# Performance work log

Measured on AMD Instinct MI355X. Metric: run time of the kernel, lower is better.

The kernel has to match this reference:

```python
import jax, jax.numpy as jnp
import numpy as np

NUM_CODES = 1024
CODE_DIM = 256
COMMIT_W = 0.25
EPS = 1e-5
ENT_LO, ENT_HI = 0.5, 0.9
ENT_W = 0.1
VAR_FLOOR = 0.05
VAR_W = 1e-3
DECORR_W = 1e-3


def setup_inputs() -> dict:
    key = jax.random.key(0)
    k1, k2, k3 = jax.random.split(key, 3)
    inputs = jax.random.normal(k1, (16, 2048, CODE_DIM), dtype=jnp.float32)
    weight = jax.random.normal(k2, (NUM_CODES, CODE_DIM), dtype=jnp.float32) * 0.1
    usage_counts = jax.random.uniform(k3, (NUM_CODES,), dtype=jnp.float32)
    return {"inputs": inputs, "weight": weight, "usage_counts": usage_counts}


def reference(inputs, weight, usage_counts):
    K, D = weight.shape
    flat = inputs.reshape(-1, D)  # [N, D]
    # squared euclidean distances [N, K]
    dist = (flat ** 2).sum(axis=1, keepdims=True) - 2.0 * flat @ weight.T + (weight ** 2).sum(axis=1)
    idx = jnp.argmin(dist, axis=1)  # [N]
    quant = weight[idx].reshape(inputs.shape)

    commitment_loss = COMMIT_W * jnp.mean((jax.lax.stop_gradient(quant) - inputs) ** 2)
    # straight-through estimator
    quant_ste = inputs + jax.lax.stop_gradient(quant - inputs)

    # usage entropy regularizer
    probs = usage_counts + EPS
    probs = probs / jnp.maximum(probs.sum(), EPS * K)
    usage_entropy = -jnp.sum(probs * jnp.log(probs + EPS)) / np.log(float(K)).astype(np.float32)
    gap = jnp.where(usage_entropy < ENT_LO, ENT_LO - usage_entropy,
                    jnp.where(usage_entropy > ENT_HI, usage_entropy - ENT_HI, 0.0))
    entropy_loss = ENT_W * gap ** 2

    # variance floor penalty on codebook
    variance = jnp.var(weight, axis=0)
    variance_loss = VAR_W * jnp.mean(jax.nn.relu(VAR_FLOOR - variance))

    # decorrelation penalty
    wc = weight - weight.mean(axis=0, keepdims=True)
    cov = wc.T @ wc / float(K)  # [D, D]
    off_diag = cov - jnp.diag(jnp.diag(cov))
    decorrelation_loss = DECORR_W * jnp.mean(off_diag ** 2)

    total_loss = commitment_loss + entropy_loss + variance_loss + decorrelation_loss
    indices = idx.reshape(inputs.shape[:-1])
    return (quant_ste, indices, total_loss, commitment_loss, entropy_loss,
            variance_loss, decorrelation_loss, usage_entropy)
```

## Files before the change

kernel.cpp:

```cpp
#include <hip/hip_runtime.h>
#include <math.h>

#define DIMS   256
#define KCODES 1024
#define NTOT   32768
#define TAU    0.002f

typedef __bf16 bf16x8 __attribute__((ext_vector_type(8)));
typedef float  f32x4  __attribute__((ext_vector_type(4)));

typedef const void __attribute__((address_space(1))) glb_cv;
typedef void __attribute__((address_space(3))) lds_v;

__device__ __forceinline__ void gload_lds16(const void* g, void* l) {
  __builtin_amdgcn_global_load_lds((glb_cv*)g, (lds_v*)l, 16, 0, 0);
}

#define WS_COMMIT   0
#define WS_FLAGCNT  1
#define WS_DECORR   2
#define WS_COLSUM   16
#define WS_COLSQ    272
#define WS_WSQ      1024
#define WS_XSQ      2048
#define WS_FLAGS    34816
#define WS_CAND1    67584
#define WS_CAND2    329728
#define WS_CANDI    591872
#define WS_WP       854016

#define OUT_Q    0
#define OUT_IDX  8388608
#define OUT_SCAL 8421376

__global__ __launch_bounds__(256) void pack_kernel(const float* __restrict__ src,
                                                   __bf16* __restrict__ dst,
                                                   float* __restrict__ sqOut) {
  int tid = threadIdx.x;
  int row = blockIdx.x * 64 + (tid >> 2);
  int kg = tid & 3;
  int rb = row >> 7, rl = row & 127;
  int p1 = kg ^ (rl & 7);
  float sq = 0.f;
  #pragma unroll
  for (int kt = 0; kt < 8; kt++) {
    const float* s = src + (size_t)row * DIMS + kt * 32 + kg * 8;
    float4 u = *(const float4*)s;
    float4 v = *(const float4*)(s + 4);
    float f[8] = {u.x, u.y, u.z, u.w, v.x, v.y, v.z, v.w};
    bf16x8 hi, lo;
    #pragma unroll
    for (int e = 0; e < 8; e++) {
      __bf16 h = (__bf16)f[e];
      hi[e] = h;
      lo[e] = (__bf16)(f[e] - (float)h);
      sq = fmaf(f[e], f[e], sq);
    }
    size_t base = ((size_t)(rb * 8 + kt) * 128 + rl) * 64;
    *(bf16x8*)&dst[base + p1 * 8] = hi;
    *(bf16x8*)&dst[base + (p1 ^ 4) * 8] = lo;
  }
  sq += __shfl_xor(sq, 1);
  sq += __shfl_xor(sq, 2);
  if (kg == 0) sqOut[row] = sq;
}

__global__ __launch_bounds__(256) void colstats_kernel(const float* __restrict__ W, float* ws) {
  int d = threadIdx.x;
  int r0 = blockIdx.x * 32;
  float s = 0.f, sq = 0.f;
  #pragma unroll 8
  for (int k = 0; k < 32; k++) {
    float v = W[(size_t)(r0 + k) * DIMS + d];
    s += v;
    sq = fmaf(v, v, sq);
  }
  atomicAdd(&ws[WS_COLSUM + d], s);
  atomicAdd(&ws[WS_COLSQ + d], sq);
}

__global__ __launch_bounds__(256) void pass1_kernel(const __bf16* __restrict__ Xp,
                                                    const __bf16* __restrict__ Wp,
                                                    float* ws) {
  __shared__ __align__(16) char smem[65536];
  __shared__ float wsqs[128];
  float* d1L = (float*)smem;
  float* d2L = (float*)(smem + 1024);
  int*   i1L = (int*)(smem + 2048);

  int tid = threadIdx.x;
  int lane = tid & 63, wave = tid >> 6;
  int waveM = wave >> 1, waveN = wave & 1;
  int quad = lane >> 4, col = lane & 15;
  int l = blockIdx.x;
  int bm = (l & 7) * 32 + ((l >> 3) & 31);
  int bn = l >> 8;
  int rowBase = bm * 128, cb = bn * 128;

  if (tid < 128) wsqs[tid] = ws[WS_WSQ + cb + tid];

  f32x4 acc[4][4];
  #pragma unroll
  for (int i = 0; i < 4; i++)
    #pragma unroll
    for (int j = 0; j < 4; j++) acc[i][j] = (f32x4){0.f, 0.f, 0.f, 0.f};

  const char* abase = (const char*)(Xp + ((size_t)(bm * 8) << 13));
  const char* bbase = (const char*)(Wp + ((size_t)(bn * 8) << 13));
  int llo = wave * 4096 + lane * 16;

  #pragma unroll
  for (int i = 0; i < 4; i++) {
    int off = wave * 4096 + i * 1024;
    gload_lds16(abase + off + lane * 16, smem + off);
    gload_lds16(bbase + off + lane * 16, smem + 32768 + off);
  }
  (void)llo;

  for (int kt = 0; kt < 8; kt++) {
    __syncthreads();
    if (kt < 7) {
      int b = (kt + 1) & 1;
      const char* as = abase + (size_t)(kt + 1) * 16384;
      const char* bs = bbase + (size_t)(kt + 1) * 16384;
      #pragma unroll
      for (int i = 0; i < 4; i++) {
        int off = wave * 4096 + i * 1024;
        gload_lds16(as + off + lane * 16, smem + b * 16384 + off);
        gload_lds16(bs + off + lane * 16, smem + 32768 + b * 16384 + off);
      }
    }
    const __bf16* Ab = (const __bf16*)(smem + (kt & 1) * 16384);
    const __bf16* Bb = (const __bf16*)(smem + 32768 + (kt & 1) * 16384);

    bf16x8 ah[4], al[4];
    #pragma unroll
    for (int mt = 0; mt < 4; mt++) {
      int r = waveM * 64 + mt * 16 + col;
      int ph = quad ^ (r & 7);
      ah[mt] = *(const bf16x8*)&Ab[r * 64 + ph * 8];
      al[mt] = *(const bf16x8*)&Ab[r * 64 + (ph ^ 4) * 8];
    }
    #pragma unroll
    for (int nt = 0; nt < 4; nt++) {
      int r = waveN * 64 + nt * 16 + col;
      int ph = quad ^ (r & 7);
      bf16x8 bh = *(const bf16x8*)&Bb[r * 64 + ph * 8];
      bf16x8 bl = *(const bf16x8*)&Bb[r * 64 + (ph ^ 4) * 8];
      #pragma unroll
      for (int mt = 0; mt < 4; mt++) {
        acc[mt][nt] = __builtin_amdgcn_mfma_f32_16x16x32_bf16(ah[mt], bh, acc[mt][nt], 0, 0, 0);
        acc[mt][nt] = __builtin_amdgcn_mfma_f32_16x16x32_bf16(ah[mt], bl, acc[mt][nt], 0, 0, 0);
        acc[mt][nt] = __builtin_amdgcn_mfma_f32_16x16x32_bf16(al[mt], bh, acc[mt][nt], 0, 0, 0);
      }
    }
  }

  #pragma unroll
  for (int mt = 0; mt < 4; mt++) {
    #pragma unroll
    for (int r = 0; r < 4; r++) {
      float d1 = 3.0e38f, d2 = 3.0e38f;
      int i1 = 0;
      #pragma unroll
      for (int nt = 0; nt < 4; nt++) {
        int lc = waveN * 64 + nt * 16 + col;
        float d = wsqs[lc] - 2.0f * acc[mt][nt][r];
        int g = cb + lc;
        if (d < d1) { d2 = d1; d1 = d; i1 = g; }
        else if (d < d2) d2 = d;
      }
      #pragma unroll
      for (int m = 1; m < 16; m <<= 1) {
        float od1 = __shfl_xor(d1, m);
        int oi1 = __shfl_xor(i1, m);
        float od2 = __shfl_xor(d2, m);
        if (od1 < d1 || (od1 == d1 && oi1 < i1)) {
          d2 = fminf(d1, fminf(d2, od2));
          d1 = od1; i1 = oi1;
        } else {
          d2 = fminf(od1, fminf(d2, od2));
        }
      }
      if (col == 0) {
        int lr = waveM * 64 + mt * 16 + quad * 4 + r;
        d1L[lr * 2 + waveN] = d1;
        d2L[lr * 2 + waveN] = d2;
        i1L[lr * 2 + waveN] = i1;
      }
    }
  }
  __syncthreads();
  if (tid < 128) {
    float a1 = d1L[tid * 2], a2 = d2L[tid * 2];
    int ai = i1L[tid * 2];
    float b1 = d1L[tid * 2 + 1], b2 = d2L[tid * 2 + 1];
    int bi = i1L[tid * 2 + 1];
    float m1, m2; int mi;
    if (b1 < a1 || (b1 == a1 && bi < ai)) { m1 = b1; mi = bi; m2 = fminf(a1, b2); }
    else { m1 = a1; mi = ai; m2 = fminf(b1, a2); }
    int o = bn * NTOT + rowBase + tid;
    ws[WS_CAND1 + o] = m1;
    ws[WS_CAND2 + o] = m2;
    ((int*)ws)[WS_CANDI + o] = mi;
  }
}

__global__ __launch_bounds__(256) void pass2_kernel(const float* __restrict__ W,
                                                    float* __restrict__ outQ,
                                                    float* __restrict__ outIdx, float* ws) {
  __shared__ int idx_s[256];
  int tid = threadIdx.x;
  int row = blockIdx.x * 256 + tid;
  const float* c1 = ws + WS_CAND1;
  const float* c2 = ws + WS_CAND2;
  const int* ci = (const int*)ws + WS_CANDI;
  float m1 = 3.0e38f, m2 = 3.0e38f;
  int mi = 0;
  #pragma unroll
  for (int b = 0; b < 8; b++) {
    int o = b * NTOT + row;
    float b1 = c1[o], b2 = c2[o];
    int bi = ci[o];
    if (b1 < m1 || (b1 == m1 && bi < mi)) { m2 = fminf(m1, b2); m1 = b1; mi = bi; }
    else { m2 = fminf(m2, b1); }
  }
  outIdx[row] = (float)mi;
  idx_s[tid] = mi;
  int* wsI = (int*)ws;
  if (m2 - m1 < TAU) {
    int p = atomicAdd(&wsI[WS_FLAGCNT], 1);
    wsI[WS_FLAGS + p] = row;
  }
  float partial = ws[WS_XSQ + row] + m1;
  #pragma unroll
  for (int m = 32; m >= 1; m >>= 1) partial += __shfl_xor(partial, m);
  if ((tid & 63) == 0) atomicAdd(&ws[WS_COMMIT], partial);
  __syncthreads();
  int wave = tid >> 6, lane = tid & 63;
  int rowBase = blockIdx.x * 256;
  for (int i = 0; i < 64; i++) {
    int rl = wave * 64 + i;
    int ix = idx_s[rl];
    float4 v = ((const float4*)(W + (size_t)ix * DIMS))[lane];
    ((float4*)(outQ + (size_t)(rowBase + rl) * DIMS))[lane] = v;
  }
}

__global__ __launch_bounds__(256) void cov_kernel(const float* __restrict__ W, float* ws) {
  __shared__ float wi_s[4][KCODES];
  __shared__ float red[4];
  int tid = threadIdx.x;
  int i0 = blockIdx.x * 4;
  int rr = tid >> 2, c = tid & 3;
  #pragma unroll
  for (int b = 0; b < 16; b++) {
    int row = b * 64 + rr;
    wi_s[c][row] = W[(size_t)row * DIMS + i0 + c];
  }
  __syncthreads();
  int j = tid;
  float a0 = 0.f, a1 = 0.f, a2 = 0.f, a3 = 0.f;
  for (int k = 0; k < KCODES; k += 4) {
    #pragma unroll
    for (int u = 0; u < 4; u++) {
      float wj = W[(size_t)(k + u) * DIMS + j];
      a0 = fmaf(wi_s[0][k + u], wj, a0);
      a1 = fmaf(wi_s[1][k + u], wj, a1);
      a2 = fmaf(wi_s[2][k + u], wj, a2);
      a3 = fmaf(wi_s[3][k + u], wj, a3);
    }
  }
  const float inv = 1.0f / 1024.0f;
  float mj = ws[WS_COLSUM + j] * inv;
  float dots[4] = {a0, a1, a2, a3};
  float v = 0.f;
  #pragma unroll
  for (int r = 0; r < 4; r++) {
    float mi = ws[WS_COLSUM + i0 + r] * inv;
    float cc = dots[r] * inv - mi * mj;
    if (i0 + r != j) v = fmaf(cc, cc, v);
  }
  #pragma unroll
  for (int m = 32; m >= 1; m >>= 1) v += __shfl_xor(v, m);
  if ((j & 63) == 0) red[j >> 6] = v;
  __syncthreads();
  if (j == 0) atomicAdd(&ws[WS_DECORR], (red[0] + red[1]) + (red[2] + red[3]));
}

__global__ __launch_bounds__(256) void refine_kernel(const float* __restrict__ X,
                                                     const float* __restrict__ W,
                                                     float* __restrict__ outQ,
                                                     float* __restrict__ outIdx, float* ws) {
  __shared__ float xs[DIMS];
  __shared__ double dm[256];
  __shared__ int im[256];
  __shared__ int chosen;
  const int* wsI = (const int*)ws;
  int cnt = wsI[WS_FLAGCNT];
  const int* list = wsI + WS_FLAGS;
  int tid = threadIdx.x;
  for (int f = blockIdx.x; f < cnt; f += gridDim.x) {
    int row = list[f];
    __syncthreads();
    if (tid < 64) ((float4*)xs)[tid] = ((const float4*)(X + (size_t)row * DIMS))[tid];
    __syncthreads();
    double bd = 1.0e300;
    int bi = 0;
    for (int jj = 0; jj < 4; jj++) {
      int c = tid + 256 * jj;
      double a0 = 0.0, a1 = 0.0, a2 = 0.0, a3 = 0.0;
      const float* wr = W + (size_t)c * DIMS;
      #pragma unroll 4
      for (int d4 = 0; d4 < 64; d4++) {
        float4 w = ((const float4*)wr)[d4];
        float4 x = ((const float4*)xs)[d4];
        double e0 = (double)x.x - (double)w.x;
        double e1 = (double)x.y - (double)w.y;
        double e2 = (double)x.z - (double)w.z;
        double e3 = (double)x.w - (double)w.w;
        a0 += e0 * e0; a1 += e1 * e1; a2 += e2 * e2; a3 += e3 * e3;
      }
      double s = (a0 + a1) + (a2 + a3);
      if (s < bd) { bd = s; bi = c; }
    }
    dm[tid] = bd; im[tid] = bi;
    __syncthreads();
    for (int st = 128; st >= 1; st >>= 1) {
      if (tid < st) {
        if (dm[tid + st] < dm[tid] || (dm[tid + st] == dm[tid] && im[tid + st] < im[tid])) {
          dm[tid] = dm[tid + st]; im[tid] = im[tid + st];
        }
      }
      __syncthreads();
    }
    if (tid == 0) { chosen = im[0]; outIdx[row] = (float)im[0]; }
    __syncthreads();
    int ix = chosen;
    if (tid < 64)
      ((float4*)(outQ + (size_t)row * DIMS))[tid] = ((const float4*)(W + (size_t)ix * DIMS))[tid];
  }
}

__global__ __launch_bounds__(256) void finalize_kernel(const float* __restrict__ U, float* ws,
                                                       float* __restrict__ out) {
  __shared__ float red[256];
  int tid = threadIdx.x;
  float s = 0.f;
  for (int e = tid; e < KCODES; e += 256) s += U[e] + 1e-5f;
  red[tid] = s;
  __syncthreads();
  for (int st = 128; st >= 1; st >>= 1) {
    if (tid < st) red[tid] += red[tid + st];
    __syncthreads();
  }
  float S = red[0];
  __syncthreads();
  float denom = fmaxf(S, 1e-5f * 1024.0f);
  float h = 0.f;
  for (int e = tid; e < KCODES; e += 256) {
    float p = (U[e] + 1e-5f) / denom;
    h += p * logf(p + 1e-5f);
  }
  red[tid] = h;
  __syncthreads();
  for (int st = 128; st >= 1; st >>= 1) {
    if (tid < st) red[tid] += red[tid + st];
    __syncthreads();
  }
  float H = -red[0] / 6.93147180559945f;
  __syncthreads();
  float m = ws[WS_COLSUM + tid] * (1.0f / 1024.0f);
  float var = ws[WS_COLSQ + tid] * (1.0f / 1024.0f) - m * m;
  float r = 0.05f - var;
  red[tid] = r > 0.f ? r : 0.f;
  __syncthreads();
  for (int st = 128; st >= 1; st >>= 1) {
    if (tid < st) red[tid] += red[tid + st];
    __syncthreads();
  }
  if (tid == 0) {
    float varloss = 1e-3f * (red[0] / 256.0f);
    float gap = H < 0.5f ? (0.5f - H) : (H > 0.9f ? (H - 0.9f) : 0.0f);
    float entloss = 0.1f * gap * gap;
    float commit = 0.25f * ws[WS_COMMIT] / 8388608.0f;
    float dec = 1e-3f * ws[WS_DECORR] / 65536.0f;
    float* sc = out + OUT_SCAL;
    sc[0] = commit + entloss + varloss + dec;
    sc[1] = commit;
    sc[2] = entloss;
    sc[3] = varloss;
    sc[4] = dec;
    sc[5] = H;
  }
}

extern "C" void kernel_launch(void* const* d_in, const int* in_sizes, int n_in, void* d_out,
                              int out_size, void* d_ws, size_t ws_size, hipStream_t stream) {
  const float* X = (const float*)d_in[0];
  const float* W = (const float*)d_in[1];
  const float* U = (const float*)d_in[2];
  float* out = (float*)d_out;
  float* ws = (float*)d_ws;
  __bf16* Xp = (__bf16*)(out + OUT_Q);
  __bf16* Wp = (__bf16*)(ws + WS_WP);

  hipMemsetAsync(d_ws, 0, 2112, stream);
  pack_kernel<<<NTOT / 64, 256, 0, stream>>>(X, Xp, ws + WS_XSQ);
  pack_kernel<<<KCODES / 64, 256, 0, stream>>>(W, Wp, ws + WS_WSQ);
  colstats_kernel<<<32, 256, 0, stream>>>(W, ws);
  pass1_kernel<<<2048, 256, 0, stream>>>(Xp, Wp, ws);
  pass2_kernel<<<NTOT / 256, 256, 0, stream>>>(W, out + OUT_Q, out + OUT_IDX, ws);
  cov_kernel<<<64, 256, 0, stream>>>(W, ws);
  refine_kernel<<<512, 256, 0, stream>>>(X, W, out + OUT_Q, out + OUT_IDX, ws);
  finalize_kernel<<<1, 256, 0, stream>>>(U, ws, out);
}
```

Baseline: 260.5 us.

## Fuse prep kernels, load codebook fragments directly to registers, tighten refine threshold

Merges the two pack launches and the column-stats launch into one prep kernel. The codebook is now packed in MFMA-fragment order, so pass1 reads its B operands straight from global memory into registers instead of staging them through LDS. This halves pass1's LDS footprint so more blocks can fit per CU (launch bounds set to 3). The ambiguity threshold TAU is also lowered, so fewer rows are flagged for exact refinement, which shrinks refine work at the cost of a tighter margin on bf16 split precision.

```diff
diff --git a/kernel.cpp b/kernel.cpp
--- a/kernel.cpp
+++ b/kernel.cpp
@@ -4,7 +4,7 @@
 #define DIMS   256
 #define KCODES 1024
 #define NTOT   32768
-#define TAU    0.002f
+#define TAU    4.0e-4f
 
 typedef __bf16 bf16x8 __attribute__((ext_vector_type(8)));
 typedef float  f32x4  __attribute__((ext_vector_type(4)));
@@ -33,60 +33,94 @@
 #define OUT_IDX  8388608
 #define OUT_SCAL 8421376
 
-__global__ __launch_bounds__(256) void pack_kernel(const float* __restrict__ src,
-                                                   __bf16* __restrict__ dst,
-                                                   float* __restrict__ sqOut) {
-  int tid = threadIdx.x;
-  int row = blockIdx.x * 64 + (tid >> 2);
-  int kg = tid & 3;
-  int rb = row >> 7, rl = row & 127;
-  int p1 = kg ^ (rl & 7);
-  float sq = 0.f;
-  #pragma unroll
-  for (int kt = 0; kt < 8; kt++) {
-    const float* s = src + (size_t)row * DIMS + kt * 32 + kg * 8;
-    float4 u = *(const float4*)s;
-    float4 v = *(const float4*)(s + 4);
-    float f[8] = {u.x, u.y, u.z, u.w, v.x, v.y, v.z, v.w};
-    bf16x8 hi, lo;
-    #pragma unroll
-    for (int e = 0; e < 8; e++) {
-      __bf16 h = (__bf16)f[e];
-      hi[e] = h;
-      lo[e] = (__bf16)(f[e] - (float)h);
-      sq = fmaf(f[e], f[e], sq);
-    }
-    size_t base = ((size_t)(rb * 8 + kt) * 128 + rl) * 64;
-    *(bf16x8*)&dst[base + p1 * 8] = hi;
-    *(bf16x8*)&dst[base + (p1 ^ 4) * 8] = lo;
-  }
-  sq += __shfl_xor(sq, 1);
-  sq += __shfl_xor(sq, 2);
-  if (kg == 0) sqOut[row] = sq;
-}
-
-__global__ __launch_bounds__(256) void colstats_kernel(const float* __restrict__ W, float* ws) {
-  int d = threadIdx.x;
-  int r0 = blockIdx.x * 32;
-  float s = 0.f, sq = 0.f;
-  #pragma unroll 8
-  for (int k = 0; k < 32; k++) {
-    float v = W[(size_t)(r0 + k) * DIMS + d];
-    s += v;
-    sq = fmaf(v, v, sq);
-  }
-  atomicAdd(&ws[WS_COLSUM + d], s);
-  atomicAdd(&ws[WS_COLSQ + d], sq);
-}
-
-__global__ __launch_bounds__(256) void pass1_kernel(const __bf16* __restrict__ Xp,
-                                                    const __bf16* __restrict__ Wp,
-                                                    float* ws) {
-  __shared__ __align__(16) char smem[65536];
+__global__ __launch_bounds__(256) void prep_kernel(const float* __restrict__ X,
+                                                   const float* __restrict__ W,
+                                                   __bf16* __restrict__ Xp,
+                                                   __bf16* __restrict__ Wp2,
+                                                   float* ws) {
+  int b = blockIdx.x;
+  int tid = threadIdx.x;
+  if (b < 512) {
+    int row = b * 64 + (tid >> 2);
+    int kg = tid & 3;
+    int rb = row >> 7, rl = row & 127;
+    int p1 = kg ^ (rl & 7);
+    float sq = 0.f;
+    #pragma unroll
+    for (int kt = 0; kt < 8; kt++) {
+      const float* s = X + (size_t)row * DIMS + kt * 32 + kg * 8;
+      float4 u = *(const float4*)s;
+      float4 v = *(const float4*)(s + 4);
+      float f[8] = {u.x, u.y, u.z, u.w, v.x, v.y, v.z, v.w};
+      bf16x8 hi, lo;
+      #pragma unroll
+      for (int e = 0; e < 8; e++) {
+        __bf16 h = (__bf16)f[e];
+        hi[e] = h;
+        lo[e] = (__bf16)(f[e] - (float)h);
+        sq = fmaf(f[e], f[e], sq);
+      }
+      size_t base = ((size_t)(rb * 8 + kt) * 128 + rl) * 64;
+      *(bf16x8*)&Xp[base + p1 * 8] = hi;
+      *(bf16x8*)&Xp[base + (p1 ^ 4) * 8] = lo;
+    }
+    sq += __shfl_xor(sq, 1);
+    sq += __shfl_xor(sq, 2);
+    if (kg == 0) ws[WS_XSQ + row] = sq;
+  } else if (b < 544) {
+    int b2 = b - 512;
+    int g = b2 * 32 + (tid >> 3);
+    int kt = tid & 7;
+    int bn = g >> 7, c = g & 127;
+    int wn = c >> 6, nt = (c >> 4) & 3, lcol = c & 15;
+    size_t hibase = ((((size_t)(bn * 8 + kt) * 2 + wn) * 4 + nt) * 2 + 0) * 512;
+    size_t lobase = hibase + 512;
+    const float* s = W + (size_t)g * DIMS + kt * 32;
+    float sq = 0.f;
+    #pragma unroll
+    for (int kq = 0; kq < 4; kq++) {
+      float4 u = *(const float4*)(s + kq * 8);
+      float4 v = *(const float4*)(s + kq * 8 + 4);
+      float f[8] = {u.x, u.y, u.z, u.w, v.x, v.y, v.z, v.w};
+      bf16x8 hi, lo;
+      #pragma unroll
+      for (int e = 0; e < 8; e++) {
+        __bf16 h = (__bf16)f[e];
+        hi[e] = h;
+        lo[e] = (__bf16)(f[e] - (float)h);
+        sq = fmaf(f[e], f[e], sq);
+      }
+      size_t off = (size_t)(kq * 16 + lcol) * 8;
+      *(bf16x8*)&Wp2[hibase + off] = hi;
+      *(bf16x8*)&Wp2[lobase + off] = lo;
+    }
+    sq += __shfl_xor(sq, 1);
+    sq += __shfl_xor(sq, 2);
+    sq += __shfl_xor(sq, 4);
+    if (kt == 0) ws[WS_WSQ + g] = sq;
+  } else {
+    int d = tid;
+    int r0 = (b - 544) * 128;
+    float s = 0.f, sq = 0.f;
+    #pragma unroll 8
+    for (int k = 0; k < 128; k++) {
+      float v = W[(size_t)(r0 + k) * DIMS + d];
+      s += v;
+      sq = fmaf(v, v, sq);
+    }
+    atomicAdd(&ws[WS_COLSUM + d], s);
+    atomicAdd(&ws[WS_COLSQ + d], sq);
+  }
+}
+
+__global__ __launch_bounds__(256, 3) void pass1_kernel(const __bf16* __restrict__ Xp,
+                                                       const __bf16* __restrict__ Wp2,
+                                                       float* ws) {
+  __shared__ __align__(16) char asmem[32768];
   __shared__ float wsqs[128];
-  float* d1L = (float*)smem;
-  float* d2L = (float*)(smem + 1024);
-  int*   i1L = (int*)(smem + 2048);
+  __shared__ float d1L[256];
+  __shared__ float d2L[256];
+  __shared__ int   i1L[256];
 
   int tid = threadIdx.x;
   int lane = tid & 63, wave = tid >> 6;
@@ -106,33 +140,30 @@
     for (int j = 0; j < 4; j++) acc[i][j] = (f32x4){0.f, 0.f, 0.f, 0.f};
 
   const char* abase = (const char*)(Xp + ((size_t)(bm * 8) << 13));
-  const char* bbase = (const char*)(Wp + ((size_t)(bn * 8) << 13));
-  int llo = wave * 4096 + lane * 16;
+  const __bf16* wbase = Wp2 + ((size_t)(bn * 8) * 2 + waveN) * 4096;
 
   #pragma unroll
   for (int i = 0; i < 4; i++) {
     int off = wave * 4096 + i * 1024;
-    gload_lds16(abase + off + lane * 16, smem + off);
-    gload_lds16(bbase + off + lane * 16, smem + 32768 + off);
-  }
-  (void)llo;
+    gload_lds16(abase + off + lane * 16, asmem + off);
+  }
 
   for (int kt = 0; kt < 8; kt++) {
     __syncthreads();
+    const __bf16* wp = wbase + (size_t)kt * 8192;
+    bf16x8 bfr[8];
+    #pragma unroll
+    for (int f = 0; f < 8; f++) bfr[f] = *(const bf16x8*)(wp + f * 512 + lane * 8);
     if (kt < 7) {
-      int b = (kt + 1) & 1;
       const char* as = abase + (size_t)(kt + 1) * 16384;
-      const char* bs = bbase + (size_t)(kt + 1) * 16384;
+      int bsel = (kt + 1) & 1;
       #pragma unroll
       for (int i = 0; i < 4; i++) {
         int off = wave * 4096 + i * 1024;
-        gload_lds16(as + off + lane * 16, smem + b * 16384 + off);
-        gload_lds16(bs + off + lane * 16, smem + 32768 + b * 16384 + off);
-      }
-    }
-    const __bf16* Ab = (const __bf16*)(smem + (kt & 1) * 16384);
-    const __bf16* Bb = (const __bf16*)(smem + 32768 + (kt & 1) * 16384);
-
+        gload_lds16(as + off + lane * 16, asmem + bsel * 16384 + off);
+      }
+    }
+    const __bf16* Ab = (const __bf16*)(asmem + (kt & 1) * 16384);
     bf16x8 ah[4], al[4];
     #pragma unroll
     for (int mt = 0; mt < 4; mt++) {
@@ -143,15 +174,11 @@
     }
     #pragma unroll
     for (int nt = 0; nt < 4; nt++) {
-      int r = waveN * 64 + nt * 16 + col;
-      int ph = quad ^ (r & 7);
-      bf16x8 bh = *(const bf16x8*)&Bb[r * 64 + ph * 8];
-      bf16x8 bl = *(const bf16x8*)&Bb[r * 64 + (ph ^ 4) * 8];
       #pragma unroll
       for (int mt = 0; mt < 4; mt++) {
-        acc[mt][nt] = __builtin_amdgcn_mfma_f32_16x16x32_bf16(ah[mt], bh, acc[mt][nt], 0, 0, 0);
-        acc[mt][nt] = __builtin_amdgcn_mfma_f32_16x16x32_bf16(ah[mt], bl, acc[mt][nt], 0, 0, 0);
-        acc[mt][nt] = __builtin_amdgcn_mfma_f32_16x16x32_bf16(al[mt], bh, acc[mt][nt], 0, 0, 0);
+        acc[mt][nt] = __builtin_amdgcn_mfma_f32_16x16x32_bf16(ah[mt], bfr[nt * 2], acc[mt][nt], 0, 0, 0);
+        acc[mt][nt] = __builtin_amdgcn_mfma_f32_16x16x32_bf16(ah[mt], bfr[nt * 2 + 1], acc[mt][nt], 0, 0, 0);
+        acc[mt][nt] = __builtin_amdgcn_mfma_f32_16x16x32_bf16(al[mt], bfr[nt * 2], acc[mt][nt], 0, 0, 0);
       }
     }
   }
@@ -239,6 +266,7 @@
   __syncthreads();
   int wave = tid >> 6, lane = tid & 63;
   int rowBase = blockIdx.x * 256;
+  #pragma unroll 4
   for (int i = 0; i < 64; i++) {
     int rl = wave * 64 + i;
     int ix = idx_s[rl];
@@ -403,13 +431,11 @@
   float* out = (float*)d_out;
   float* ws = (float*)d_ws;
   __bf16* Xp = (__bf16*)(out + OUT_Q);
-  __bf16* Wp = (__bf16*)(ws + WS_WP);
+  __bf16* Wp2 = (__bf16*)(ws + WS_WP);
 
   hipMemsetAsync(d_ws, 0, 2112, stream);
-  pack_kernel<<<NTOT / 64, 256, 0, stream>>>(X, Xp, ws + WS_XSQ);
-  pack_kernel<<<KCODES / 64, 256, 0, stream>>>(W, Wp, ws + WS_WSQ);
-  colstats_kernel<<<32, 256, 0, stream>>>(W, ws);
-  pass1_kernel<<<2048, 256, 0, stream>>>(Xp, Wp, ws);
+  prep_kernel<<<552, 256, 0, stream>>>(X, W, Xp, Wp2, ws);
+  pass1_kernel<<<2048, 256, 0, stream>>>(Xp, Wp2, ws);
   pass2_kernel<<<NTOT / 256, 256, 0, stream>>>(W, out + OUT_Q, out + OUT_IDX, ws);
   cov_kernel<<<64, 256, 0, stream>>>(W, ws);
   refine_kernel<<<512, 256, 0, stream>>>(X, W, out + OUT_Q, out + OUT_IDX, ws);
```

Result: faster. 246.2 us (-5.5%).
